# Performance work log

Measured on AMD Instinct MI355X. Metric: run time of the kernel, lower is better.

## Reference

```python
import jax, jax.numpy as jnp
import numpy as np

IN_F, OUT_F, RANK = 4096, 4096, 16
ALPHA = 32.0
SCALING = ALPHA / RANK


def setup_inputs() -> dict:
    key = jax.random.key(0)
    kx, kw, ka, kb = jax.random.split(key, 4)
    x = jax.random.normal(kx, (4, 2048, IN_F), dtype=jnp.float32)
    # base linear weight [out, in] (kaiming-uniform-like scale)
    bound_w = 1.0 / np.sqrt(IN_F)
    W = jax.random.uniform(kw, (OUT_F, IN_F), minval=-bound_w, maxval=bound_w, dtype=jnp.float32)
    # lora_A [rank, in]: kaiming uniform; lora_B [out, rank]: nonzero for testing
    bound_a = np.sqrt(6.0 / IN_F) / np.sqrt(1.0 + 5.0)
    lora_A = jax.random.uniform(ka, (RANK, IN_F), minval=-bound_a, maxval=bound_a, dtype=jnp.float32)
    lora_B = jax.random.normal(kb, (OUT_F, RANK), dtype=jnp.float32) * 0.02
    return {"x": x, "W": W, "lora_A": lora_A, "lora_B": lora_B}


def reference(x, W, lora_A, lora_B):
    # base: x @ W^T  -> [b, s, out]
    base = jnp.einsum("bsi,oi->bso", x, W)
    # low-rank path: (x @ A^T) @ B^T * scaling (dropout p=0 -> identity)
    r = jnp.einsum("bsi,ri->bsr", x, lora_A)  # [b, s, rank]
    lora = jnp.einsum("bsr,or->bso", r, lora_B) * SCALING
    return base + lora
```

## Files before the change

kernel.cpp:

```cpp
#include <hip/hip_runtime.h>
#include <stdint.h>
#include <stddef.h>

#define IN_F    4096
#define OUT_F   4096
#define MTOK    8192
#define RANK    16
#define SCALING 2.0f

typedef __attribute__((ext_vector_type(8))) short          bf16x8;
typedef __attribute__((ext_vector_type(4))) float          f32x4;
typedef __attribute__((ext_vector_type(4))) float          fl4;
typedef __attribute__((ext_vector_type(4))) unsigned short u16x4;
typedef __attribute__((ext_vector_type(8))) unsigned short u16x8;

static __device__ __forceinline__ unsigned short f2bf(float f) {
  union { float f; uint32_t u; } v; v.f = f;
  return (unsigned short)((v.u + 0x7fffu + ((v.u >> 16) & 1u)) >> 16);
}

static __device__ __forceinline__ void gload16(const void* g, void* l) {
  __builtin_amdgcn_global_load_lds(
      (const __attribute__((address_space(1))) uint32_t*)g,
      (__attribute__((address_space(3))) uint32_t*)l,
      16, 0, 0);
}

__global__ void prep_kernel(const float* __restrict__ x,
                            const float* __restrict__ W,
                            const float* __restrict__ lA,
                            const float* __restrict__ lB,
                            unsigned short* __restrict__ Weff,
                            unsigned short* __restrict__ xb) {
  __shared__ float Bs[RANK];
  if (blockIdx.x < OUT_F) {
    const int o = blockIdx.x;
    if (threadIdx.x < RANK) Bs[threadIdx.x] = lB[o * RANK + threadIdx.x] * SCALING;
    __syncthreads();
    for (int c = threadIdx.x * 4; c < IN_F; c += 256 * 4) {
      fl4 w = *(const fl4*)(W + (size_t)o * IN_F + c);
#pragma unroll
      for (int r = 0; r < RANK; ++r) {
        const float b = Bs[r];
        const fl4 a = *(const fl4*)(lA + (size_t)r * IN_F + c);
        w[0] += b * a[0]; w[1] += b * a[1]; w[2] += b * a[2]; w[3] += b * a[3];
      }
      u16x4 p;
      p[0] = f2bf(w[0]); p[1] = f2bf(w[1]); p[2] = f2bf(w[2]); p[3] = f2bf(w[3]);
      *(u16x4*)(Weff + (size_t)o * IN_F + c) = p;
    }
  } else {
    const size_t i = ((size_t)(blockIdx.x - OUT_F) * 256 + threadIdx.x) * 8;
    const fl4 a = *(const fl4*)(x + i);
    const fl4 b = *(const fl4*)(x + i + 4);
    u16x8 p;
    p[0] = f2bf(a[0]); p[1] = f2bf(a[1]); p[2] = f2bf(a[2]); p[3] = f2bf(a[3]);
    p[4] = f2bf(b[0]); p[5] = f2bf(b[1]); p[6] = f2bf(b[2]); p[7] = f2bf(b[3]);
    *(u16x8*)(xb + i) = p;
  }
}

__global__ __launch_bounds__(512, 2) void gemm8p_kernel(
    const unsigned short* __restrict__ X,
    const unsigned short* __restrict__ Wf,
    float* __restrict__ Out) {
  __shared__ char lds[131072];
  const int tid  = threadIdx.x;
  const int lane = tid & 63;
  const int wave = tid >> 6;
  const int wr = wave >> 2;
  const int wc = wave & 3;
  const int fr = lane & 15;
  const int fq = lane >> 4;

  const int bid = blockIdx.x;
  const int tm  = (bid & 7) * 4 + ((bid >> 3) & 3);
  const int tn  = bid >> 5;
  const int m0 = tm << 8;
  const int n0 = tn << 8;

  const unsigned short* Ag = X  + (size_t)m0 * IN_F;
  const unsigned short* Bg = Wf + (size_t)n0 * IN_F;

  const int rIW = lane >> 3;
  const int csw = ((lane & 7) ^ rIW) << 3;

  const int aBase = wr * 16384 + fr * 128;
  const int bBase = 65536 + (wc >> 1) * 16384 + (wc & 1) * 8192 + fr * 128;
  const int cA0 = (fq << 4) ^ ((fr & 7) << 4);
  const int cA1 = cA0 ^ 64;

#define STAGE_A(C, BUF, K) do {                                                \
    const int _rh = (C) * 64 + (wave & 3) * 16;                                \
    const int _r0 = (wave >> 2) * 128 + _rh + rIW;                             \
    char* _d = lds + (BUF) * 32768 + (wave >> 2) * 16384 + _rh * 128 +         \
               (lane << 4);                                                    \
    gload16(Ag + (size_t)_r0 * IN_F + (K) + csw, _d);                          \
    gload16(Ag + (size_t)(_r0 + 8) * IN_F + (K) + csw, _d + 1024);             \
  } while (0)

#define STAGE_B(C, BUF, K) do {                                                \
    const int _s  = wave >> 1;                                                 \
    const int _rh = (_s & 1) * 64 + (C) * 32 + (wave & 1) * 16;                \
    const int _r0 = (_s >> 1) * 128 + _rh + rIW;                               \
    char* _d = lds + 65536 + (BUF) * 32768 + (_s >> 1) * 16384 + _rh * 128 +   \
               (lane << 4);                                                    \
    gload16(Bg + (size_t)_r0 * IN_F + (K) + csw, _d);                          \
    gload16(Bg + (size_t)(_r0 + 8) * IN_F + (K) + csw, _d + 1024);             \
  } while (0)

#define LDA(BUF, M, KK) (*(const bf16x8*)(lds + (BUF) * 32768 + aBase + (M) * 2048 + (KK)))
#define LDB(BUF, N, KK) (*(const bf16x8*)(lds + (BUF) * 32768 + bBase + (N) * 2048 + (KK)))

#define MFMA_Q(MB, NB, BR)                                                     \
  _Pragma("unroll")                                                            \
  for (int mi = 0; mi < 4; ++mi)                                               \
    _Pragma("unroll")                                                          \
    for (int ni = 0; ni < 2; ++ni) {                                           \
      acc[(MB)+mi][(NB)+ni] = __builtin_amdgcn_mfma_f32_16x16x32_bf16(a[mi*2],   BR[ni*2],   acc[(MB)+mi][(NB)+ni], 0, 0, 0); \
      acc[(MB)+mi][(NB)+ni] = __builtin_amdgcn_mfma_f32_16x16x32_bf16(a[mi*2+1], BR[ni*2+1], acc[(MB)+mi][(NB)+ni], 0, 0, 0); \
    }

#define TILE(BU, NB, KN, PF)                                                   \
  do {                                                                         \
                                                    \
    if (PF) { STAGE_B(0, NB, KN);                                              \
              asm volatile("s_waitcnt vmcnt(4)" ::: "memory"); }               \
    else    { asm volatile("s_waitcnt vmcnt(2)" ::: "memory"); }               \
    __builtin_amdgcn_s_barrier();                                              \
    _Pragma("unroll")                                                          \
    for (int mi = 0; mi < 4; ++mi) { a[mi*2] = LDA(BU, mi, cA0); a[mi*2+1] = LDA(BU, mi, cA1); } \
    _Pragma("unroll")                                                          \
    for (int ni = 0; ni < 2; ++ni) { b0[ni*2] = LDB(BU, ni, cA0); b0[ni*2+1] = LDB(BU, ni, cA1); } \
    __builtin_amdgcn_s_setprio(1);                                             \
    MFMA_Q(0, 0, b0)                                                           \
    __builtin_amdgcn_s_setprio(0);                                             \
    _Pragma("unroll")                                                          \
    for (int ni = 0; ni < 2; ++ni) { b1[ni*2] = LDB(BU, 2+ni, cA0); b1[ni*2+1] = LDB(BU, 2+ni, cA1); } \
    __builtin_amdgcn_s_barrier();                                              \
                                                    \
    if (PF) { STAGE_B(1, NB, KN);                                              \
              asm volatile("s_waitcnt vmcnt(4)" ::: "memory"); }               \
    else    { asm volatile("s_waitcnt vmcnt(0)" ::: "memory"); }               \
    __builtin_amdgcn_s_barrier();                                              \
    __builtin_amdgcn_s_setprio(1);                                             \
    MFMA_Q(0, 2, b1)                                                           \
    __builtin_amdgcn_s_setprio(0);                                             \
    _Pragma("unroll")                                                          \
    for (int mi = 0; mi < 4; ++mi) { a[mi*2] = LDA(BU, 4+mi, cA0); a[mi*2+1] = LDA(BU, 4+mi, cA1); } \
    __builtin_amdgcn_s_barrier();                                              \
                                                    \
    if (PF) STAGE_A(0, NB, KN);                                                \
    __builtin_amdgcn_s_barrier();                                              \
    __builtin_amdgcn_s_setprio(1);                                             \
    MFMA_Q(4, 2, b1)                                                           \
    __builtin_amdgcn_s_setprio(0);                                             \
    __builtin_amdgcn_s_barrier();                                              \
                                                    \
    if (PF) STAGE_A(1, NB, KN);                                                \
    __builtin_amdgcn_s_barrier();                                              \
    __builtin_amdgcn_s_setprio(1);                                             \
    MFMA_Q(4, 0, b0)                                                           \
    __builtin_amdgcn_s_setprio(0);                                             \
    __builtin_amdgcn_s_barrier();                                              \
  } while (0)

  f32x4 acc[8][4];
#pragma unroll
  for (int i = 0; i < 8; ++i)
#pragma unroll
    for (int j = 0; j < 4; ++j) acc[i][j] = (f32x4){0.f, 0.f, 0.f, 0.f};

  bf16x8 a[8], b0[4], b1[4];

  STAGE_B(0, 0, 0); STAGE_B(1, 0, 0); STAGE_A(0, 0, 0); STAGE_A(1, 0, 0);

  for (int tt = 0; tt < 32; ++tt) {
    const int k1 = (tt << 7) + 64;
    const int k2 = k1 + 64;
    TILE(0, 1, k1, true);
    TILE(1, 0, k2, (k2 < IN_F));
  }

#pragma unroll
  for (int mi = 0; mi < 8; ++mi) {
    const int row0 = m0 + wr * 128 + mi * 16 + fq * 4;
#pragma unroll
    for (int ni = 0; ni < 4; ++ni) {
      const int col = n0 + wc * 64 + ni * 16 + fr;
#pragma unroll
      for (int j = 0; j < 4; ++j)
        Out[(size_t)(row0 + j) * OUT_F + col] = acc[mi][ni][j];
    }
  }
#undef STAGE_A
#undef STAGE_B
#undef LDA
#undef LDB
#undef MFMA_Q
#undef TILE
}

__global__ __launch_bounds__(256) void gemm_f32x_kernel(
    const float* __restrict__ X,
    const unsigned short* __restrict__ Weff,
    float* __restrict__ Out) {
  __shared__ unsigned short As[128][32];
  __shared__ unsigned short Bs[128][32];

  const int tid  = threadIdx.x;
  const int lane = tid & 63;
  const int wave = tid >> 6;
  const int wr = wave >> 1, wc = wave & 1;
  const int fr = lane & 15, fq = lane >> 4;

  const int bid = blockIdx.x;
  const int m0 = (bid & 63) * 128;
  const int n0 = (bid >> 6) * 128;

  f32x4 acc[4][4];
#pragma unroll
  for (int i = 0; i < 4; ++i)
#pragma unroll
    for (int j = 0; j < 4; ++j) acc[i][j] = (f32x4){0.f, 0.f, 0.f, 0.f};

  const int srow = tid >> 2;
  const int sseg = tid & 3;

  for (int k0 = 0; k0 < IN_F; k0 += 32) {
    if (k0) __syncthreads();
    {
      const unsigned short* gB = Weff + (size_t)(n0 + srow) * IN_F + k0 + sseg * 8;
      gload16(gB, &Bs[srow][sseg * 8]);
      gload16(gB + (size_t)64 * IN_F, &Bs[64 + srow][sseg * 8]);
    }
#pragma unroll
    for (int it = 0; it < 4; ++it) {
      const int c   = tid + it * 256;
      const int row = c >> 3;
      const int c4  = (c & 7) * 4;
      const fl4 v = *(const fl4*)(X + (size_t)(m0 + row) * IN_F + k0 + c4);
      u16x4 p;
      p[0] = f2bf(v[0]); p[1] = f2bf(v[1]); p[2] = f2bf(v[2]); p[3] = f2bf(v[3]);
      *(u16x4*)&As[row][c4] = p;
    }
    __syncthreads();

    bf16x8 af[4], bfm[4];
#pragma unroll
    for (int m = 0; m < 4; ++m)
      af[m] = *(const bf16x8*)&As[wr * 64 + m * 16 + fr][fq * 8];
#pragma unroll
    for (int n = 0; n < 4; ++n)
      bfm[n] = *(const bf16x8*)&Bs[wc * 64 + n * 16 + fr][fq * 8];
#pragma unroll
    for (int m = 0; m < 4; ++m)
#pragma unroll
      for (int n = 0; n < 4; ++n)
        acc[m][n] = __builtin_amdgcn_mfma_f32_16x16x32_bf16(af[m], bfm[n], acc[m][n], 0, 0, 0);
  }

#pragma unroll
  for (int m = 0; m < 4; ++m) {
    const int row0 = m0 + wr * 64 + m * 16 + fq * 4;
#pragma unroll
    for (int n = 0; n < 4; ++n) {
      const int col = n0 + wc * 64 + n * 16 + fr;
#pragma unroll
      for (int j = 0; j < 4; ++j)
        Out[(size_t)(row0 + j) * OUT_F + col] = acc[m][n][j];
    }
  }
}

__global__ void lora_r_kernel(const float* __restrict__ x,
                              const float* __restrict__ lA,
                              float* __restrict__ r) {
  const int idx = blockIdx.x * 256 + threadIdx.x;
  const int m = idx / RANK, rr = idx % RANK;
  float acc = 0.f;
  for (int k = 0; k < IN_F; ++k)
    acc += x[(size_t)m * IN_F + k] * lA[(size_t)rr * IN_F + k];
  r[idx] = acc * SCALING;
}

__global__ void naive_out_kernel(const float* __restrict__ x,
                                 const float* __restrict__ W,
                                 const float* __restrict__ lB,
                                 const float* __restrict__ r,
                                 float* __restrict__ out) {
  const size_t idx = (size_t)blockIdx.x * 256 + threadIdx.x;
  const int m = (int)(idx / OUT_F), n = (int)(idx % OUT_F);
  float acc = 0.f;
  for (int k = 0; k < IN_F; ++k)
    acc += x[(size_t)m * IN_F + k] * W[(size_t)n * IN_F + k];
#pragma unroll
  for (int rr = 0; rr < RANK; ++rr)
    acc += r[(size_t)m * RANK + rr] * lB[(size_t)n * RANK + rr];
  out[idx] = acc;
}

extern "C" void kernel_launch(void* const* d_in, const int* in_sizes, int n_in,
                              void* d_out, int out_size, void* d_ws, size_t ws_size,
                              hipStream_t stream) {
  const float* x  = (const float*)d_in[0];
  const float* W  = (const float*)d_in[1];
  const float* lA = (const float*)d_in[2];
  const float* lB = (const float*)d_in[3];
  float* out = (float*)d_out;

  const size_t weff_bytes = (size_t)OUT_F * IN_F * 2;
  const size_t xb_bytes   = (size_t)MTOK * IN_F * 2;

  if (ws_size >= weff_bytes + xb_bytes) {
    unsigned short* Weff = (unsigned short*)d_ws;
    unsigned short* xb   = (unsigned short*)((char*)d_ws + weff_bytes);
    const int conv_blocks = (int)((MTOK * (size_t)IN_F) / (256 * 8));
    prep_kernel<<<OUT_F + conv_blocks, 256, 0, stream>>>(x, W, lA, lB, Weff, xb);
    gemm8p_kernel<<<(MTOK / 256) * (OUT_F / 256), 512, 0, stream>>>(xb, Weff, out);
  } else if (ws_size >= weff_bytes) {
    unsigned short* Weff = (unsigned short*)d_ws;
    prep_kernel<<<OUT_F, 256, 0, stream>>>(x, W, lA, lB, Weff, (unsigned short*)0);
    gemm_f32x_kernel<<<(MTOK / 128) * (OUT_F / 128), 256, 0, stream>>>(x, Weff, out);
  } else {
    float* r = (float*)d_ws;
    lora_r_kernel<<<(MTOK * RANK) / 256, 256, 0, stream>>>(x, lA, r);
    naive_out_kernel<<<(size_t)MTOK * OUT_F / 256, 256, 0, stream>>>(x, W, lB, r, out);
  }
}
```

Before: 303.6 us.

## Cut GEMM barriers per tile and merge four weight rows per prep block

The GEMM tile loop goes from eight workgroup barriers per half-tile to three. Global-to-LDS staging and the vmcnt waits now sit between the MFMA groups, wrapped in sched_barrier fences so the compiler cannot move work across them. Separately, the prep kernel folds the LoRA update into four W rows per block, so each lora_A load is reused four times. The risk is a race: STAGE_A writes into LDS while other waves may still be reading the A fragments without a barrier between them, which could corrupt results.

```diff
diff --git a/kernel.cpp b/kernel.cpp
--- a/kernel.cpp
+++ b/kernel.cpp
@@ -25,6 +25,11 @@
       (__attribute__((address_space(3))) uint32_t*)l,
       16, 0, 0);
 }
+
+#define SBAR() __builtin_amdgcn_sched_barrier(0)
+#define BARRIER() do { SBAR(); __builtin_amdgcn_s_barrier(); SBAR(); } while (0)
+
+#define MERGE_BLKS (OUT_F / 4)
 
 __global__ void prep_kernel(const float* __restrict__ x,
                             const float* __restrict__ W,
@@ -32,25 +37,43 @@
                             const float* __restrict__ lB,
                             unsigned short* __restrict__ Weff,
                             unsigned short* __restrict__ xb) {
-  __shared__ float Bs[RANK];
-  if (blockIdx.x < OUT_F) {
-    const int o = blockIdx.x;
-    if (threadIdx.x < RANK) Bs[threadIdx.x] = lB[o * RANK + threadIdx.x] * SCALING;
+  __shared__ float Bs[4][RANK];
+  if (blockIdx.x < MERGE_BLKS) {
+    const int o0 = blockIdx.x * 4;
+    if (threadIdx.x < 4 * RANK)
+      Bs[threadIdx.x >> 4][threadIdx.x & 15] =
+          lB[o0 * RANK + threadIdx.x] * SCALING;
     __syncthreads();
-    for (int c = threadIdx.x * 4; c < IN_F; c += 256 * 4) {
-      fl4 w = *(const fl4*)(W + (size_t)o * IN_F + c);
+#pragma unroll
+    for (int it = 0; it < 4; ++it) {
+      const int c = threadIdx.x * 4 + it * 1024;
+      fl4 w0 = *(const fl4*)(W + (size_t)(o0 + 0) * IN_F + c);
+      fl4 w1 = *(const fl4*)(W + (size_t)(o0 + 1) * IN_F + c);
+      fl4 w2 = *(const fl4*)(W + (size_t)(o0 + 2) * IN_F + c);
+      fl4 w3 = *(const fl4*)(W + (size_t)(o0 + 3) * IN_F + c);
 #pragma unroll
       for (int r = 0; r < RANK; ++r) {
-        const float b = Bs[r];
         const fl4 a = *(const fl4*)(lA + (size_t)r * IN_F + c);
-        w[0] += b * a[0]; w[1] += b * a[1]; w[2] += b * a[2]; w[3] += b * a[3];
+        const float b0 = Bs[0][r], b1 = Bs[1][r], b2 = Bs[2][r], b3 = Bs[3][r];
+#pragma unroll
+        for (int e = 0; e < 4; ++e) {
+          w0[e] += b0 * a[e]; w1[e] += b1 * a[e];
+          w2[e] += b2 * a[e]; w3[e] += b3 * a[e];
+        }
       }
-      u16x4 p;
-      p[0] = f2bf(w[0]); p[1] = f2bf(w[1]); p[2] = f2bf(w[2]); p[3] = f2bf(w[3]);
-      *(u16x4*)(Weff + (size_t)o * IN_F + c) = p;
+      u16x4 p0, p1, p2, p3;
+#pragma unroll
+      for (int e = 0; e < 4; ++e) {
+        p0[e] = f2bf(w0[e]); p1[e] = f2bf(w1[e]);
+        p2[e] = f2bf(w2[e]); p3[e] = f2bf(w3[e]);
+      }
+      *(u16x4*)(Weff + (size_t)(o0 + 0) * IN_F + c) = p0;
+      *(u16x4*)(Weff + (size_t)(o0 + 1) * IN_F + c) = p1;
+      *(u16x4*)(Weff + (size_t)(o0 + 2) * IN_F + c) = p2;
+      *(u16x4*)(Weff + (size_t)(o0 + 3) * IN_F + c) = p3;
     }
   } else {
-    const size_t i = ((size_t)(blockIdx.x - OUT_F) * 256 + threadIdx.x) * 8;
+    const size_t i = ((size_t)(blockIdx.x - MERGE_BLKS) * 256 + threadIdx.x) * 8;
     const fl4 a = *(const fl4*)(x + i);
     const fl4 b = *(const fl4*)(x + i + 4);
     u16x8 p;
@@ -123,11 +146,10 @@
 
 #define TILE(BU, NB, KN, PF)                                                   \
   do {                                                                         \
-                                                    \
     if (PF) { STAGE_B(0, NB, KN);                                              \
               asm volatile("s_waitcnt vmcnt(4)" ::: "memory"); }               \
     else    { asm volatile("s_waitcnt vmcnt(2)" ::: "memory"); }               \
-    __builtin_amdgcn_s_barrier();                                              \
+    BARRIER();                                                                 \
     _Pragma("unroll")                                                          \
     for (int mi = 0; mi < 4; ++mi) { a[mi*2] = LDA(BU, mi, cA0); a[mi*2+1] = LDA(BU, mi, cA1); } \
     _Pragma("unroll")                                                          \
@@ -137,32 +159,24 @@
     __builtin_amdgcn_s_setprio(0);                                             \
     _Pragma("unroll")                                                          \
     for (int ni = 0; ni < 2; ++ni) { b1[ni*2] = LDB(BU, 2+ni, cA0); b1[ni*2+1] = LDB(BU, 2+ni, cA1); } \
-    __builtin_amdgcn_s_barrier();                                              \
-                                                    \
-    if (PF) { STAGE_B(1, NB, KN);                                              \
-              asm volatile("s_waitcnt vmcnt(4)" ::: "memory"); }               \
-    else    { asm volatile("s_waitcnt vmcnt(0)" ::: "memory"); }               \
-    __builtin_amdgcn_s_barrier();                                              \
+    if (PF) STAGE_B(1, NB, KN);                                                \
     __builtin_amdgcn_s_setprio(1);                                             \
     MFMA_Q(0, 2, b1)                                                           \
     __builtin_amdgcn_s_setprio(0);                                             \
+    if (PF) { asm volatile("s_waitcnt vmcnt(4)" ::: "memory"); }               \
+    else    { asm volatile("s_waitcnt vmcnt(0)" ::: "memory"); }               \
+    BARRIER();                                                                 \
     _Pragma("unroll")                                                          \
     for (int mi = 0; mi < 4; ++mi) { a[mi*2] = LDA(BU, 4+mi, cA0); a[mi*2+1] = LDA(BU, 4+mi, cA1); } \
-    __builtin_amdgcn_s_barrier();                                              \
-                                                    \
     if (PF) STAGE_A(0, NB, KN);                                                \
-    __builtin_amdgcn_s_barrier();                                              \
     __builtin_amdgcn_s_setprio(1);                                             \
     MFMA_Q(4, 2, b1)                                                           \
     __builtin_amdgcn_s_setprio(0);                                             \
-    __builtin_amdgcn_s_barrier();                                              \
-                                                    \
     if (PF) STAGE_A(1, NB, KN);                                                \
-    __builtin_amdgcn_s_barrier();                                              \
     __builtin_amdgcn_s_setprio(1);                                             \
     MFMA_Q(4, 0, b0)                                                           \
     __builtin_amdgcn_s_setprio(0);                                             \
-    __builtin_amdgcn_s_barrier();                                              \
+    BARRIER();                                                                 \
   } while (0)
 
   f32x4 acc[8][4];
@@ -316,11 +330,11 @@
     unsigned short* Weff = (unsigned short*)d_ws;
     unsigned short* xb   = (unsigned short*)((char*)d_ws + weff_bytes);
     const int conv_blocks = (int)((MTOK * (size_t)IN_F) / (256 * 8));
-    prep_kernel<<<OUT_F + conv_blocks, 256, 0, stream>>>(x, W, lA, lB, Weff, xb);
+    prep_kernel<<<MERGE_BLKS + conv_blocks, 256, 0, stream>>>(x, W, lA, lB, Weff, xb);
     gemm8p_kernel<<<(MTOK / 256) * (OUT_F / 256), 512, 0, stream>>>(xb, Weff, out);
   } else if (ws_size >= weff_bytes) {
     unsigned short* Weff = (unsigned short*)d_ws;
-    prep_kernel<<<OUT_F, 256, 0, stream>>>(x, W, lA, lB, Weff, (unsigned short*)0);
+    prep_kernel<<<MERGE_BLKS, 256, 0, stream>>>(x, W, lA, lB, Weff, (unsigned short*)0);
     gemm_f32x_kernel<<<(MTOK / 128) * (OUT_F / 128), 256, 0, stream>>>(x, Weff, out);
   } else {
     float* r = (float*)d_ws;
```

Result: no change. 299.7 us (-1.3%).
